# Kernel tuning notes

Measured on AMD Instinct MI355X. Metric: run time of the kernel, lower is better.

## Reference

```python
import jax, jax.numpy as jnp
import numpy as np

NUM_RELATIONS = 4
N_NODES = 20000
N_EDGES = 320000
F_IN = 128
HID = 128
EMB = 128


def _rgcn_conv(x, src, dst, edge_type, edge_weight, W, root, bias):
    """One WeightedRGCNConv layer.
    x: [N, in]; W: [R, in, out]; root: [in, out]; bias: [out].
    Math identical to m = einsum('ei,eio->eo', x[src], W[edge_type]) but computed
    as R grouped matmuls to avoid materializing the [E, in, out] weight copy.
    """
    xj = x[src]  # [E, in] gather
    m = jnp.zeros((xj.shape[0], W.shape[2]), dtype=x.dtype)
    for r in range(W.shape[0]):  # fixed small relation count
        mask = (edge_type == r).astype(x.dtype)[:, None]
        m = m + mask * (xj @ W[r])
    m = m * edge_weight[:, None]
    out = jax.ops.segment_sum(m, dst, num_segments=x.shape[0])  # scatter_add
    return out + x @ root + bias


def setup_inputs() -> dict:
    key = jax.random.key(0)
    ks = jax.random.split(key, 10)
    return {
        "x": jax.random.normal(ks[0], (N_NODES, F_IN), dtype=jnp.float32),
        "edge_index": jax.random.randint(ks[1], (2, N_EDGES), 0, N_NODES, dtype=jnp.int64 if jax.config.jax_enable_x64 else jnp.int32).astype(jnp.int32),
        "edge_type": jax.random.randint(ks[2], (N_EDGES,), 0, NUM_RELATIONS).astype(jnp.int32),
        "edge_weight": jax.random.uniform(ks[3], (N_EDGES,), dtype=jnp.float32),
        "W1": jax.random.normal(ks[4], (NUM_RELATIONS, F_IN, HID), dtype=jnp.float32) * 0.05,
        "root1": jax.random.normal(ks[5], (F_IN, HID), dtype=jnp.float32) * 0.05,
        "b1": jax.random.normal(ks[6], (HID,), dtype=jnp.float32) * 0.05,
        "W2": jax.random.normal(ks[7], (NUM_RELATIONS, HID, EMB), dtype=jnp.float32) * 0.05,
        "root2": jax.random.normal(ks[8], (HID, EMB), dtype=jnp.float32) * 0.05,
        "b2": jax.random.normal(ks[9], (EMB,), dtype=jnp.float32) * 0.05,
    }


def reference(x, edge_index, edge_type, edge_weight, W1, root1, b1, W2, root2, b2):
    src, dst = edge_index[0], edge_index[1]
    # min-max normalize edge weights (as in RGCN.forward)
    ew = (edge_weight - edge_weight.min()) / (edge_weight.max() - edge_weight.min() + 1e-08)
    h = jax.nn.relu(_rgcn_conv(x, src, dst, edge_type, ew, W1, root1, b1))
    h = _rgcn_conv(h, src, dst, edge_type, ew, W2, root2, b2)
    return h
```

## Files before the change

### kernel.cpp

```cpp
#include <hip/hip_runtime.h>

#define NN 20000
#define NE 320000
#define FD 128
#define KTOT 640
#define BM 32

typedef float f32x4 __attribute__((ext_vector_type(4)));
typedef __bf16 bf16x8 __attribute__((ext_vector_type(8)));

__device__ __forceinline__ unsigned f2ord(float f) {
  unsigned u = __float_as_uint(f);
  return (u & 0x80000000u) ? ~u : (u | 0x80000000u);
}
__device__ __forceinline__ float ord2f(unsigned u) {
  return (u & 0x80000000u) ? __uint_as_float(u & 0x7FFFFFFFu) : __uint_as_float(~u);
}
__device__ __forceinline__ unsigned pkbf(float a, float b) {
  union { __bf16 h[2]; unsigned u; } p;
  p.h[0] = (__bf16)a; p.h[1] = (__bf16)b; return p.u;
}

__global__ void init_kernel(unsigned* mm, int* deg,
                            const float* __restrict__ x, unsigned* __restrict__ xb) {
  int i = blockIdx.x * blockDim.x + threadIdx.x;
  if (i == 0) { mm[0] = 0xFFFFFFFFu; mm[1] = 0u; }
  if (i < NN) deg[i] = 0;
  if (i < NN * FD / 4) {
    float4 v = *(const float4*)(x + (size_t)i * 4);
    uint2 p;
    p.x = pkbf(v.x, v.y);
    p.y = pkbf(v.z, v.w);
    *(uint2*)(xb + (size_t)i * 2) = p;
  }
}

__global__ void histmm_kernel(const int* __restrict__ dst, const float* __restrict__ ew,
                              int* deg, unsigned* mm) {
  __shared__ unsigned smn[256], smx[256];
  unsigned lmn = 0xFFFFFFFFu, lmx = 0u;
  for (int i = blockIdx.x * blockDim.x + threadIdx.x; i < NE; i += gridDim.x * blockDim.x) {
    atomicAdd(&deg[dst[i]], 1);
    unsigned o = f2ord(ew[i]);
    lmn = (o < lmn) ? o : lmn;
    lmx = (o > lmx) ? o : lmx;
  }
  smn[threadIdx.x] = lmn; smx[threadIdx.x] = lmx;
  __syncthreads();
  for (int s = 128; s > 0; s >>= 1) {
    if (threadIdx.x < s) {
      unsigned a = smn[threadIdx.x], b = smn[threadIdx.x + s];
      smn[threadIdx.x] = (b < a) ? b : a;
      unsigned c = smx[threadIdx.x], d = smx[threadIdx.x + s];
      smx[threadIdx.x] = (d > c) ? d : c;
    }
    __syncthreads();
  }
  if (threadIdx.x == 0) { atomicMin(&mm[0], smn[0]); atomicMax(&mm[1], smx[0]); }
}

__global__ void scan_kernel(const int* __restrict__ deg, int* offs, int* cursor) {
  __shared__ int part[1024];
  const int CH = (NN + 1023) / 1024;
  int t = threadIdx.x;
  int b = t * CH;
  int e = (b + CH < NN) ? (b + CH) : NN;
  int s = 0;
  for (int i = b; i < e; ++i) s += deg[i];
  part[t] = s;
  __syncthreads();
  for (int off = 1; off < 1024; off <<= 1) {
    int v = part[t];
    int add = (t >= off) ? part[t - off] : 0;
    __syncthreads();
    part[t] = v + add;
    __syncthreads();
  }
  int excl = (t == 0) ? 0 : part[t - 1];
  for (int i = b; i < e; ++i) { offs[i] = excl; cursor[i] = excl; excl += deg[i]; }
  if (t == 1023) offs[NN] = part[1023];
}

__global__ void fill_kernel(const int* __restrict__ src, const int* __restrict__ dst,
                            const int* __restrict__ et, const float* __restrict__ ew,
                            const unsigned* __restrict__ mm, int* cursor,
                            int2* __restrict__ ed) {
  int e = blockIdx.x * blockDim.x + threadIdx.x;
  if (e >= NE) return;
  float mn = ord2f(mm[0]), mx = ord2f(mm[1]);
  float inv = 1.0f / (mx - mn + 1e-8f);
  int d = dst[e];
  int pos = atomicAdd(&cursor[d], 1);
  ed[pos] = make_int2(src[e] | (et[e] << 28), __float_as_int((ew[e] - mn) * inv));
}

__global__ void prep_wt_both(const float* __restrict__ W1, const float* __restrict__ r1,
                             const float* __restrict__ W2, const float* __restrict__ r2,
                             __bf16* __restrict__ wt1, __bf16* __restrict__ wt2) {
  int idx = blockIdx.x * blockDim.x + threadIdx.x;
  if (idx >= 2 * FD * KTOT) return;
  int which = idx / (FD * KTOT);
  int rem = idx % (FD * KTOT);
  int n = rem / KTOT, k = rem % KTOT;
  const float* W = which ? W2 : W1;
  const float* rt = which ? r2 : r1;
  __bf16* wt = which ? wt2 : wt1;
  float v = (k < 512) ? W[(size_t)k * FD + n] : rt[(size_t)(k - 512) * FD + n];
  wt[rem] = (__bf16)v;
}

template <int BF16OUT>
__global__ __launch_bounds__(512, 2) void fused_kernel(
    const unsigned* __restrict__ xb,
    const int* __restrict__ offs, const int2* __restrict__ ed,
    const __bf16* __restrict__ wt, const float* __restrict__ bias,
    float* __restrict__ outf, __bf16* __restrict__ outb) {
  __shared__ unsigned As32[BM * 320];
  int tid = threadIdx.x;
  int wave = tid >> 6, lane = tid & 63;
  int wr = wave >> 2, wc = wave & 3;
  int m0 = blockIdx.x * BM;
  int rl = wr * 16 + (lane & 15);
  int kfe = (lane >> 4) * 8;
  int c0 = wc * 32 + (lane & 15);
  const f32x4 zz = {0.f, 0.f, 0.f, 0.f};

  unsigned rowpack = 0, colpack0 = 0, colpack1 = 0;
  {
    if (tid < 256) {
      int row = tid >> 3;
      int wl = (tid & 7) * 2;
      unsigned val = pkbf((float)row * 0.03125f, (float)row * 0.03125f);
      int sw2 = (row & 7) << 2;
      As32[row * 320 + (wl ^ sw2)] = val;
      As32[row * 320 + ((wl + 1) ^ sw2)] = val;
    }
    __syncthreads();
    const char* Arow = (const char*)As32 + rl * 1280;
    int swb = (rl & 7) << 4;
    bf16x8 pa = *(const bf16x8*)(Arow + ((kfe * 2) ^ swb));
    bf16x8 ones, bp0, bp1;
#pragma unroll
    for (int i = 0; i < 8; ++i) ones[i] = (__bf16)1.0f;
    __bf16 c0v = (__bf16)((float)c0 * 0.0078125f);
    __bf16 c1v = (__bf16)((float)(c0 + 16) * 0.0078125f);
#pragma unroll
    for (int i = 0; i < 8; ++i) { bp0[i] = c0v; bp1[i] = c1v; }
    f32x4 P1 = __builtin_amdgcn_mfma_f32_16x16x32_bf16(pa, ones, zz, 0, 0, 0);
    f32x4 P2a = __builtin_amdgcn_mfma_f32_16x16x32_bf16(ones, bp0, zz, 0, 0, 0);
    f32x4 P2b = __builtin_amdgcn_mfma_f32_16x16x32_bf16(ones, bp1, zz, 0, 0, 0);
#pragma unroll
    for (int j = 0; j < 4; ++j) {
      rowpack |= ((unsigned)(int)(P1[j] + 0.5f)) << (8 * j);
      colpack0 |= ((unsigned)(int)(P2a[j] * 4.0f + 0.5f)) << (8 * j);
      colpack1 |= ((unsigned)(int)(P2b[j] * 4.0f + 0.5f)) << (8 * j);
    }
    __syncthreads();
  }

#define LOADP(E, P0, P1)                                                \
  do {                                                                  \
    int s_ = (E).x & 0x0FFFFFFF;                                        \
    unsigned u_ = xb[(size_t)s_ * 64 + lane];                           \
    P0 = __uint_as_float(u_ << 16);                                     \
    P1 = __uint_as_float(u_ & 0xFFFF0000u);                             \
  } while (0)
#define ACCP(E, P0, P1)                                                 \
  do {                                                                  \
    float w_ = __int_as_float((E).y);                                   \
    unsigned r_ = ((unsigned)(E).x) >> 28;                              \
    float w0_ = (r_ == 0) ? w_ : 0.f, w1_ = (r_ == 1) ? w_ : 0.f;       \
    float w2_ = (r_ == 2) ? w_ : 0.f, w3_ = (r_ == 3) ? w_ : 0.f;       \
    a00 += w0_ * (P0); a01 += w0_ * (P1);                               \
    a10 += w1_ * (P0); a11 += w1_ * (P1);                               \
    a20 += w2_ * (P0); a21 += w2_ * (P1);                               \
    a30 += w3_ * (P0); a31 += w3_ * (P1);                               \
  } while (0)

  for (int nl = 0; nl < 4; ++nl) {
    int nloc = (wave << 2) + nl;
    int node = m0 + nloc;
    int beg = offs[node], end = offs[node + 1];
    float a00 = 0.f, a01 = 0.f, a10 = 0.f, a11 = 0.f;
    float a20 = 0.f, a21 = 0.f, a30 = 0.f, a31 = 0.f;
    int j = beg;
    for (; j + 4 <= end; j += 4) {
      int2 e0 = ed[j], e1 = ed[j + 1], e2 = ed[j + 2], e3 = ed[j + 3];
      float p00, p01, p10, p11, p20, p21, p30, p31;
      LOADP(e0, p00, p01); LOADP(e1, p10, p11);
      LOADP(e2, p20, p21); LOADP(e3, p30, p31);
      ACCP(e0, p00, p01); ACCP(e1, p10, p11);
      ACCP(e2, p20, p21); ACCP(e3, p30, p31);
    }
    for (; j < end; ++j) {
      int2 e = ed[j];
      float p0, p1;
      LOADP(e, p0, p1);
      ACCP(e, p0, p1);
    }
    int sw2 = (nloc & 7) << 2;
    unsigned* row = As32 + nloc * 320;
    row[(0 * 64 + lane) ^ sw2] = pkbf(a00, a01);
    row[(1 * 64 + lane) ^ sw2] = pkbf(a10, a11);
    row[(2 * 64 + lane) ^ sw2] = pkbf(a20, a21);
    row[(3 * 64 + lane) ^ sw2] = pkbf(a30, a31);
    row[(4 * 64 + lane) ^ sw2] = xb[(size_t)node * 64 + lane];
  }
#undef LOADP
#undef ACCP
  __syncthreads();

  f32x4 acc0 = zz, acc1 = zz;
  const __bf16* w0p = wt + (size_t)c0 * KTOT + kfe;
  const __bf16* w1p = w0p + 16 * KTOT;
  const char* Arow = (const char*)As32 + rl * 1280;
  int swb = (rl & 7) << 4;
#pragma unroll
  for (int step = 0; step < 20; ++step) {
    int b = (step * 64 + kfe * 2) ^ swb;
    bf16x8 a = *(const bf16x8*)(Arow + b);
    bf16x8 b0 = *(const bf16x8*)(w0p + step * 32);
    bf16x8 b1 = *(const bf16x8*)(w1p + step * 32);
    acc0 = __builtin_amdgcn_mfma_f32_16x16x32_bf16(a, b0, acc0, 0, 0, 0);
    acc1 = __builtin_amdgcn_mfma_f32_16x16x32_bf16(a, b1, acc1, 0, 0, 0);
  }

#pragma unroll
  for (int j = 0; j < 4; ++j) {
    int rloc = (int)((rowpack >> (8 * j)) & 255u);
    size_t m = (size_t)(m0 + rloc);
    {
      int col = (int)((colpack0 >> (8 * j)) & 255u);
      float v = acc0[j] + bias[col];
      if (BF16OUT) outb[m * FD + col] = (__bf16)fmaxf(v, 0.f);
      else outf[m * FD + col] = v;
    }
    {
      int col = (int)((colpack1 >> (8 * j)) & 255u);
      float v = acc1[j] + bias[col];
      if (BF16OUT) outb[m * FD + col] = (__bf16)fmaxf(v, 0.f);
      else outf[m * FD + col] = v;
    }
  }
}

extern "C" void kernel_launch(void* const* d_in, const int* in_sizes, int n_in,
                              void* d_out, int out_size, void* d_ws, size_t ws_size,
                              hipStream_t stream) {
  const float* x  = (const float*)d_in[0];
  const int*   ei = (const int*)d_in[1];
  const int*   et = (const int*)d_in[2];
  const float* ew = (const float*)d_in[3];
  const float* W1 = (const float*)d_in[4];
  const float* r1 = (const float*)d_in[5];
  const float* b1 = (const float*)d_in[6];
  const float* W2 = (const float*)d_in[7];
  const float* r2 = (const float*)d_in[8];
  const float* b2 = (const float*)d_in[9];
  float* out = (float*)d_out;
  const int* src = ei;
  const int* dst = ei + NE;

  char* w = (char*)d_ws;
  size_t o = 0;
  auto take = [&](size_t bytes) -> char* {
    char* p = w + o;
    o += (bytes + 255) & ~(size_t)255;
    return p;
  };
  unsigned* mm  = (unsigned*)take(8);
  int* deg      = (int*)take((size_t)NN * 4);
  int* offs     = (int*)take((size_t)(NN + 1) * 4);
  int* cursor   = (int*)take((size_t)NN * 4);
  int2* ed      = (int2*)take((size_t)NE * 8);
  unsigned* xb  = (unsigned*)take((size_t)NN * 64 * 4);
  __bf16* h1    = (__bf16*)take((size_t)NN * FD * 2);
  __bf16* wt1   = (__bf16*)take((size_t)FD * KTOT * 2);
  __bf16* wt2   = (__bf16*)take((size_t)FD * KTOT * 2);
  (void)ws_size; (void)n_in; (void)in_sizes; (void)out_size;

  hipLaunchKernelGGL(init_kernel, dim3((NN * FD / 4 + 255) / 256), dim3(256), 0, stream,
                     mm, deg, x, xb);
  hipLaunchKernelGGL(histmm_kernel, dim3(512), dim3(256), 0, stream, dst, ew, deg, mm);
  hipLaunchKernelGGL(scan_kernel, dim3(1), dim3(1024), 0, stream, deg, offs, cursor);
  hipLaunchKernelGGL(fill_kernel, dim3((NE + 255) / 256), dim3(256), 0, stream,
                     src, dst, et, ew, mm, cursor, ed);
  hipLaunchKernelGGL(prep_wt_both, dim3((2 * FD * KTOT + 255) / 256), dim3(256), 0, stream,
                     W1, r1, W2, r2, wt1, wt2);
  hipLaunchKernelGGL((fused_kernel<1>), dim3(NN / BM), dim3(512), 0, stream,
                     xb, offs, ed, wt1, b1, (float*)nullptr, h1);
  hipLaunchKernelGGL((fused_kernel<0>), dim3(NN / BM), dim3(512), 0, stream,
                     (const unsigned*)h1, offs, ed, wt2, b2, out, (__bf16*)nullptr);
}
```

Before: 192.5 us.

## Split fused gather-GEMM into separate aggregate and GEMM kernels

Splits each layer's fused kernel in two. A standalone aggregation kernel gives each node one wavefront: it loads 8-byte bf16 vectors, splits edges between two half-waves, prefetches the next edges, and writes a 640-wide bf16 row to a global buffer. A GEMM kernel then copies that buffer into LDS and runs the MFMA loop, and the weight-transpose prep is folded into the init kernel. The aim is more parallelism and memory-level overlap in the gather, at the cost of an extra round trip to global memory for the intermediate (about 25 MB per layer) and an extra launch per layer.

```diff
diff --git a/kernel.cpp b/kernel.cpp
--- a/kernel.cpp
+++ b/kernel.cpp
@@ -21,11 +21,23 @@
   p.h[0] = (__bf16)a; p.h[1] = (__bf16)b; return p.u;
 }
 
-__global__ void init_kernel(unsigned* mm, int* deg,
-                            const float* __restrict__ x, unsigned* __restrict__ xb) {
+__global__ void prep_kernel(unsigned* mm, int* deg,
+                            const float* __restrict__ x, unsigned* __restrict__ xb,
+                            const float* __restrict__ W1, const float* __restrict__ r1,
+                            const float* __restrict__ W2, const float* __restrict__ r2,
+                            __bf16* __restrict__ wt1, __bf16* __restrict__ wt2) {
   int i = blockIdx.x * blockDim.x + threadIdx.x;
   if (i == 0) { mm[0] = 0xFFFFFFFFu; mm[1] = 0u; }
   if (i < NN) deg[i] = 0;
+  if (i < 2 * FD * KTOT) {
+    int which = i / (FD * KTOT);
+    int rem = i % (FD * KTOT);
+    int n = rem / KTOT, k = rem % KTOT;
+    const float* W = which ? W2 : W1;
+    const float* rt = which ? r2 : r1;
+    float v = (k < 512) ? W[(size_t)k * FD + n] : rt[(size_t)(k - 512) * FD + n];
+    (which ? wt2 : wt1)[rem] = (__bf16)v;
+  }
   if (i < NN * FD / 4) {
     float4 v = *(const float4*)(x + (size_t)i * 4);
     uint2 p;
@@ -94,25 +106,86 @@
   ed[pos] = make_int2(src[e] | (et[e] << 28), __float_as_int((ew[e] - mn) * inv));
 }
 
-__global__ void prep_wt_both(const float* __restrict__ W1, const float* __restrict__ r1,
-                             const float* __restrict__ W2, const float* __restrict__ r2,
-                             __bf16* __restrict__ wt1, __bf16* __restrict__ wt2) {
-  int idx = blockIdx.x * blockDim.x + threadIdx.x;
-  if (idx >= 2 * FD * KTOT) return;
-  int which = idx / (FD * KTOT);
-  int rem = idx % (FD * KTOT);
-  int n = rem / KTOT, k = rem % KTOT;
-  const float* W = which ? W2 : W1;
-  const float* rt = which ? r2 : r1;
-  __bf16* wt = which ? wt2 : wt1;
-  float v = (k < 512) ? W[(size_t)k * FD + n] : rt[(size_t)(k - 512) * FD + n];
-  wt[rem] = (__bf16)v;
-}
-
-template <int BF16OUT>
-__global__ __launch_bounds__(512, 2) void fused_kernel(
+__global__ __launch_bounds__(256) void aggregate_kernel(
     const unsigned* __restrict__ xb,
     const int* __restrict__ offs, const int2* __restrict__ ed,
+    unsigned* __restrict__ g) {
+  int node = (int)((blockIdx.x * blockDim.x + threadIdx.x) >> 6);
+  int lane = threadIdx.x & 63;
+  if (node >= NN) return;
+  int half = lane >> 5, l = lane & 31;
+  int beg = offs[node], end = offs[node + 1];
+  f32x4 a0 = {0.f, 0.f, 0.f, 0.f}, a1 = a0, a2 = a0, a3 = a0;
+
+#define GAT(E, U)                                                        \
+  do {                                                                   \
+    int s_ = (E).x & 0x0FFFFFFF;                                         \
+    U = *(const uint2*)(xb + (size_t)s_ * 64 + l * 2);                   \
+  } while (0)
+#define ACCW(E, U, WV)                                                   \
+  do {                                                                   \
+    float p0 = __uint_as_float((U).x << 16);                             \
+    float p1 = __uint_as_float((U).x & 0xFFFF0000u);                     \
+    float p2 = __uint_as_float((U).y << 16);                             \
+    float p3 = __uint_as_float((U).y & 0xFFFF0000u);                     \
+    unsigned r_ = ((unsigned)(E).x) >> 28;                               \
+    float w0 = (r_ == 0) ? (WV) : 0.f, w1 = (r_ == 1) ? (WV) : 0.f;      \
+    float w2 = (r_ == 2) ? (WV) : 0.f, w3 = (r_ == 3) ? (WV) : 0.f;      \
+    a0[0] += w0 * p0; a0[1] += w0 * p1; a0[2] += w0 * p2; a0[3] += w0 * p3; \
+    a1[0] += w1 * p0; a1[1] += w1 * p1; a1[2] += w1 * p2; a1[3] += w1 * p3; \
+    a2[0] += w2 * p0; a2[1] += w2 * p1; a2[2] += w2 * p2; a2[3] += w2 * p3; \
+    a3[0] += w3 * p0; a3[1] += w3 * p1; a3[2] += w3 * p2; a3[3] += w3 * p3; \
+  } while (0)
+
+  int j2 = beg;
+  if (j2 + 4 <= end) {
+    int2 eA = ed[j2 + half];
+    int2 eB = ed[j2 + 2 + half];
+    do {
+      uint2 uA, uB;
+      GAT(eA, uA);
+      GAT(eB, uB);
+      int2 eA2 = ed[j2 + 4 + half];
+      int2 eB2 = ed[j2 + 6 + half];
+      ACCW(eA, uA, __int_as_float(eA.y));
+      ACCW(eB, uB, __int_as_float(eB.y));
+      eA = eA2; eB = eB2;
+      j2 += 4;
+    } while (j2 + 4 <= end);
+  }
+  for (; j2 < end; j2 += 2) {
+    int je = j2 + half;
+    int2 e = ed[(je < end) ? je : (end - 1)];
+    float wv = (je < end) ? __int_as_float(e.y) : 0.f;
+    uint2 u;
+    GAT(e, u);
+    ACCW(e, u, wv);
+  }
+#undef GAT
+#undef ACCW
+
+#pragma unroll
+  for (int q = 0; q < 4; ++q) {
+    a0[q] += __shfl_xor(a0[q], 32, 64);
+    a1[q] += __shfl_xor(a1[q], 32, 64);
+    a2[q] += __shfl_xor(a2[q], 32, 64);
+    a3[q] += __shfl_xor(a3[q], 32, 64);
+  }
+
+  unsigned* row = g + (size_t)node * 320;
+  f32x4 va = half ? a2 : a0;
+  f32x4 vb = half ? a3 : a1;
+  int r01 = half * 2;
+  uint2 w0 = make_uint2(pkbf(va[0], va[1]), pkbf(va[2], va[3]));
+  *(uint2*)(row + r01 * 64 + l * 2) = w0;
+  uint2 w1 = make_uint2(pkbf(vb[0], vb[1]), pkbf(vb[2], vb[3]));
+  *(uint2*)(row + (r01 + 1) * 64 + l * 2) = w1;
+  row[256 + lane] = xb[(size_t)node * 64 + lane];
+}
+
+template <int BF16OUT>
+__global__ __launch_bounds__(512, 2) void gemm_kernel(
+    const unsigned* __restrict__ gA,
     const __bf16* __restrict__ wt, const float* __restrict__ bias,
     float* __restrict__ outf, __bf16* __restrict__ outb) {
   __shared__ unsigned As32[BM * 320];
@@ -158,56 +231,19 @@
     __syncthreads();
   }
 
-#define LOADP(E, P0, P1)                                                \
-  do {                                                                  \
-    int s_ = (E).x & 0x0FFFFFFF;                                        \
-    unsigned u_ = xb[(size_t)s_ * 64 + lane];                           \
-    P0 = __uint_as_float(u_ << 16);                                     \
-    P1 = __uint_as_float(u_ & 0xFFFF0000u);                             \
-  } while (0)
-#define ACCP(E, P0, P1)                                                 \
-  do {                                                                  \
-    float w_ = __int_as_float((E).y);                                   \
-    unsigned r_ = ((unsigned)(E).x) >> 28;                              \
-    float w0_ = (r_ == 0) ? w_ : 0.f, w1_ = (r_ == 1) ? w_ : 0.f;       \
-    float w2_ = (r_ == 2) ? w_ : 0.f, w3_ = (r_ == 3) ? w_ : 0.f;       \
-    a00 += w0_ * (P0); a01 += w0_ * (P1);                               \
-    a10 += w1_ * (P0); a11 += w1_ * (P1);                               \
-    a20 += w2_ * (P0); a21 += w2_ * (P1);                               \
-    a30 += w3_ * (P0); a31 += w3_ * (P1);                               \
-  } while (0)
-
-  for (int nl = 0; nl < 4; ++nl) {
-    int nloc = (wave << 2) + nl;
-    int node = m0 + nloc;
-    int beg = offs[node], end = offs[node + 1];
-    float a00 = 0.f, a01 = 0.f, a10 = 0.f, a11 = 0.f;
-    float a20 = 0.f, a21 = 0.f, a30 = 0.f, a31 = 0.f;
-    int j = beg;
-    for (; j + 4 <= end; j += 4) {
-      int2 e0 = ed[j], e1 = ed[j + 1], e2 = ed[j + 2], e3 = ed[j + 3];
-      float p00, p01, p10, p11, p20, p21, p30, p31;
-      LOADP(e0, p00, p01); LOADP(e1, p10, p11);
-      LOADP(e2, p20, p21); LOADP(e3, p30, p31);
-      ACCP(e0, p00, p01); ACCP(e1, p10, p11);
-      ACCP(e2, p20, p21); ACCP(e3, p30, p31);
-    }
-    for (; j < end; ++j) {
-      int2 e = ed[j];
-      float p0, p1;
-      LOADP(e, p0, p1);
-      ACCP(e, p0, p1);
-    }
-    int sw2 = (nloc & 7) << 2;
-    unsigned* row = As32 + nloc * 320;
-    row[(0 * 64 + lane) ^ sw2] = pkbf(a00, a01);
-    row[(1 * 64 + lane) ^ sw2] = pkbf(a10, a11);
-    row[(2 * 64 + lane) ^ sw2] = pkbf(a20, a21);
-    row[(3 * 64 + lane) ^ sw2] = pkbf(a30, a31);
-    row[(4 * 64 + lane) ^ sw2] = xb[(size_t)node * 64 + lane];
-  }
-#undef LOADP
-#undef ACCP
+  {
+    int row = tid >> 4;
+    int c16 = tid & 15;
+    const uint4* srcp = (const uint4*)(gA + (size_t)(m0 + row) * 320);
+    unsigned sw2 = (row & 7) << 2;
+    unsigned* dstw = As32 + row * 320;
+#pragma unroll
+    for (int jj = 0; jj < 5; ++jj) {
+      int chunk = c16 + 16 * jj;
+      uint4 v = srcp[chunk];
+      *(uint4*)(dstw + ((chunk * 4) ^ sw2)) = v;
+    }
+  }
   __syncthreads();
 
   f32x4 acc0 = zz, acc1 = zz;
@@ -272,23 +308,25 @@
   int* deg      = (int*)take((size_t)NN * 4);
   int* offs     = (int*)take((size_t)(NN + 1) * 4);
   int* cursor   = (int*)take((size_t)NN * 4);
-  int2* ed      = (int2*)take((size_t)NE * 8);
+  int2* ed      = (int2*)take((size_t)(NE + 8) * 8);
   unsigned* xb  = (unsigned*)take((size_t)NN * 64 * 4);
+  unsigned* g   = (unsigned*)take((size_t)NN * 320 * 4);
   __bf16* h1    = (__bf16*)take((size_t)NN * FD * 2);
   __bf16* wt1   = (__bf16*)take((size_t)FD * KTOT * 2);
   __bf16* wt2   = (__bf16*)take((size_t)FD * KTOT * 2);
   (void)ws_size; (void)n_in; (void)in_sizes; (void)out_size;
 
-  hipLaunchKernelGGL(init_kernel, dim3((NN * FD / 4 + 255) / 256), dim3(256), 0, stream,
-                     mm, deg, x, xb);
+  hipLaunchKernelGGL(prep_kernel, dim3((NN * FD / 4 + 255) / 256), dim3(256), 0, stream,
+                     mm, deg, x, xb, W1, r1, W2, r2, wt1, wt2);
   hipLaunchKernelGGL(histmm_kernel, dim3(512), dim3(256), 0, stream, dst, ew, deg, mm);
   hipLaunchKernelGGL(scan_kernel, dim3(1), dim3(1024), 0, stream, deg, offs, cursor);
   hipLaunchKernelGGL(fill_kernel, dim3((NE + 255) / 256), dim3(256), 0, stream,
                      src, dst, et, ew, mm, cursor, ed);
-  hipLaunchKernelGGL(prep_wt_both, dim3((2 * FD * KTOT + 255) / 256), dim3(256), 0, stream,
-                     W1, r1, W2, r2, wt1, wt2);
-  hipLaunchKernelGGL((fused_kernel<1>), dim3(NN / BM), dim3(512), 0, stream,
-                     xb, offs, ed, wt1, b1, (float*)nullptr, h1);
-  hipLaunchKernelGGL((fused_kernel<0>), dim3(NN / BM), dim3(512), 0, stream,
-                     (const unsigned*)h1, offs, ed, wt2, b2, out, (__bf16*)nullptr);
-}
+  hipLaunchKernelGGL(aggregate_kernel, dim3(NN / 4), dim3(256), 0, stream, xb, offs, ed, g);
+  hipLaunchKernelGGL((gemm_kernel<1>), dim3(NN / BM), dim3(512), 0, stream,
+                     g, wt1, b1, (float*)nullptr, h1);
+  hipLaunchKernelGGL(aggregate_kernel, dim3(NN / 4), dim3(256), 0, stream,
+                     (const unsigned*)h1, offs, ed, g);
+  hipLaunchKernelGGL((gemm_kernel<0>), dim3(NN / BM), dim3(512), 0, stream,
+                     g, wt2, b2, out, (__bf16*)nullptr);
+}
```

Measured after the change: 192.5 us. Within noise of the previous version (+0.0%).
